# Kernel tuning notes

Hardware: AMD Instinct MI355X
Metric: run time of the kernel (lower is better)

## Reference

```python
import jax, jax.numpy as jnp
import numpy as np

B, S, D, H, MULT = 4, 2048, 768, 12, 4
HD = D // H
EPS = 1e-6


def _ln(x, g, b):
    mu = jnp.mean(x, axis=-1, keepdims=True)
    var = jnp.var(x, axis=-1, keepdims=True)
    return (x - mu) * jax.lax.rsqrt(var + EPS) * g + b


def setup_inputs() -> dict:
    key = jax.random.key(0)
    ks = jax.random.split(key, 12)
    sd = 0.02
    inp = {
        "x": jax.random.normal(ks[0], (B, S, D), dtype=jnp.float32),
        "mask": jnp.ones((B, 1, 1, S), dtype=jnp.int32),
        "Wq": jax.random.normal(ks[1], (D, D), dtype=jnp.float32) * sd,
        "bq": jnp.zeros((D,), dtype=jnp.float32),
        "Wk": jax.random.normal(ks[2], (D, D), dtype=jnp.float32) * sd,
        "bk": jnp.zeros((D,), dtype=jnp.float32),
        "Wv": jax.random.normal(ks[3], (D, D), dtype=jnp.float32) * sd,
        "bv": jnp.zeros((D,), dtype=jnp.float32),
        "Wo": jax.random.normal(ks[4], (D, D), dtype=jnp.float32) * sd,
        "bo": jnp.zeros((D,), dtype=jnp.float32),
        "W1": jax.random.normal(ks[5], (D, MULT * D), dtype=jnp.float32) * sd,
        "b1": jnp.zeros((MULT * D,), dtype=jnp.float32),
        "W2": jax.random.normal(ks[6], (MULT * D, D), dtype=jnp.float32) * sd,
        "b2": jnp.zeros((D,), dtype=jnp.float32),
        "g1": jnp.ones((D,), dtype=jnp.float32),
        "be1": jnp.zeros((D,), dtype=jnp.float32),
        "g2": jnp.ones((D,), dtype=jnp.float32),
        "be2": jnp.zeros((D,), dtype=jnp.float32),
    }
    return inp


def reference(x, mask, Wq, bq, Wk, bk, Wv, bv, Wo, bo, W1, b1, W2, b2, g1, be1, g2, be2):
    scale = HD ** -0.5
    # projections -> [B,H,S,HD]
    q = (x @ Wq + bq).reshape(B, S, H, HD).transpose(0, 2, 1, 3)
    k = (x @ Wk + bk).reshape(B, S, H, HD).transpose(0, 2, 1, 3)
    v = (x @ Wv + bv).reshape(B, S, H, HD).transpose(0, 2, 1, 3)
    scores = jnp.einsum("bhqd,bhkd->bhqk", q, k) * scale
    scores = jnp.where(mask == 0, -jnp.inf, scores)
    attn = jax.nn.softmax(scores, axis=-1)
    out = jnp.einsum("bhqk,bhkd->bhqd", attn, v)
    out = out.transpose(0, 2, 1, 3).reshape(B, S, D)
    mha = out @ Wo + bo
    # residual + LN
    h = _ln(mha + x, g1, be1)
    # FFN (dropout inactive in eval; GELU exact as torch nn.GELU default)
    ff = jax.nn.gelu(h @ W1 + b1, approximate=False) @ W2 + b2
    return _ln(ff + h, g2, be2)
```

## Files before the change

kernel.cpp:

```cpp
#include <hip/hip_runtime.h>
#include <hip/hip_bf16.h>
#include <math.h>

#define B_  4
#define S_  2048
#define D_  768
#define H_  12
#define HD_ 64
#define DF_ 3072
#define BS_ (B_*S_)

#define QSCALE 0.18033688011112042f

typedef __attribute__((ext_vector_type(8))) short short8;
typedef __attribute__((ext_vector_type(4))) float f32x4;
typedef __attribute__((ext_vector_type(4))) int  int4v;

__device__ __forceinline__ unsigned short f2b(float f){
    unsigned int x = __float_as_uint(f);
    return (unsigned short)((x + 0x7fffu + ((x >> 16) & 1u)) >> 16);
}
__device__ __forceinline__ float b2f(unsigned short u){
    return __uint_as_float(((unsigned int)u) << 16);
}

typedef __attribute__((address_space(1))) void gvoid_t;
typedef __attribute__((address_space(3))) void lvoid_t;
__device__ __forceinline__ void gload_lds16(const unsigned short* g, unsigned short* l){
    __builtin_amdgcn_global_load_lds((gvoid_t*)g, (lvoid_t*)l, 16, 0, 0);
}

__global__ __launch_bounds__(256) void prep_kernel(
    const float* __restrict__ x,
    const float* __restrict__ Wq, const float* __restrict__ Wk,
    const float* __restrict__ Wv, const float* __restrict__ Wo,
    const float* __restrict__ W1, const float* __restrict__ W2,
    const float* __restrict__ bq, const float* __restrict__ bk, const float* __restrict__ bv,
    unsigned short* __restrict__ xb, unsigned short* __restrict__ wqkvT,
    unsigned short* __restrict__ woT, unsigned short* __restrict__ w1T,
    unsigned short* __restrict__ w2T, float* __restrict__ bqkv)
{
    const int NCVT = (BS_*D_)/256;
    int bid = blockIdx.x;
    if (bid < NCVT){
        int i = bid*256 + threadIdx.x;
        xb[i] = f2b(x[i]);
        return;
    }
    bid -= NCVT;
    __shared__ float t[32][33];
    const float* src; unsigned short* dst; int K, N, bx, by;
    if (bid < 4*576){
        int wsel = bid / 576, tt = bid % 576;
        bx = tt % 24; by = tt / 24; K = D_; N = D_;
        src = (wsel==0)?Wq:(wsel==1)?Wk:(wsel==2)?Wv:Wo;
        dst = (wsel<3) ? (wqkvT + (size_t)wsel*D_*D_) : woT;
    } else if (bid < 4*576 + 2304){
        int tt = bid - 4*576; bx = tt % 96; by = tt / 96; K = D_; N = DF_; src = W1; dst = w1T;
    } else if (bid < 4*576 + 2*2304){
        int tt = bid - 4*576 - 2304; bx = tt % 24; by = tt / 24; K = DF_; N = D_; src = W2; dst = w2T;
    } else {
        int i = (bid - (4*576 + 2*2304))*256 + threadIdx.x;
        if (i < 3*D_) bqkv[i] = (i < D_) ? bq[i] : (i < 2*D_) ? bk[i-D_] : bv[i-2*D_];
        return;
    }
    int tx = threadIdx.x & 31, ty = threadIdx.x >> 5;
    #pragma unroll
    for (int i = 0; i < 4; ++i)
        t[ty + i*8][tx] = src[(size_t)(by*32 + ty + i*8) * N + bx*32 + tx];
    __syncthreads();
    #pragma unroll
    for (int i = 0; i < 4; ++i)
        dst[(size_t)(bx*32 + ty + i*8) * K + by*32 + tx] = f2b(t[tx][ty + i*8]);
}

__global__ __launch_bounds__(256, 3) void gemm_tn(
    const unsigned short* __restrict__ A,
    const unsigned short* __restrict__ Bt,
    const float* __restrict__ bias,
    float* __restrict__ Cf,
    unsigned short* __restrict__ Cb,
    unsigned short* __restrict__ vtg,
    int M, int N, int K, int klen, int act)
{
    __shared__ __align__(16) unsigned short As[128*64];
    __shared__ __align__(16) unsigned short Bs[128*64];

    const int tid  = threadIdx.x;
    const int bm   = blockIdx.y, bn = blockIdx.x, bz = blockIdx.z;
    const int w    = tid >> 6, lane = tid & 63;
    const int l16  = lane & 15, quad = lane >> 4;
    const int wm   = (w >> 1) * 64, wn = (w & 1) * 64;
    const int kbeg = bz * klen;

    const unsigned short* Abase = A  + (size_t)bm * 128 * K;
    const unsigned short* Bbase = Bt + (size_t)bn * 128 * K;

    f32x4 acc[4][4] = {};

    for (int kt = kbeg; kt < kbeg + klen; kt += 64){
        #pragma unroll
        for (int c0 = 0; c0 < 4; ++c0){
            int c = tid + c0 * 256;
            int row = c >> 3, q = c & 7;
            int sw = (q ^ row) & 7;
            gload_lds16(Abase + (size_t)row * K + kt + sw*8, As + c*8);
            gload_lds16(Bbase + (size_t)row * K + kt + sw*8, Bs + c*8);
        }
        __syncthreads();

        #pragma unroll
        for (int kc = 0; kc < 2; ++kc){
            short8 af[4], bf[4];
            #pragma unroll
            for (int mi = 0; mi < 4; ++mi)
                af[mi] = *(const short8*)&As[(wm + mi*16 + l16)*64 + (((kc*4 + quad) ^ l16) & 7)*8];
            #pragma unroll
            for (int ni = 0; ni < 4; ++ni)
                bf[ni] = *(const short8*)&Bs[(wn + ni*16 + l16)*64 + (((kc*4 + quad) ^ l16) & 7)*8];
            #pragma unroll
            for (int mi = 0; mi < 4; ++mi)
                #pragma unroll
                for (int ni = 0; ni < 4; ++ni)
                    acc[mi][ni] = __builtin_amdgcn_mfma_f32_16x16x32_bf16(af[mi], bf[ni], acc[mi][ni], 0, 0, 0);
        }
        __syncthreads();
    }

    if (act == 2 && bn >= 12){
        #pragma unroll
        for (int mi = 0; mi < 4; ++mi){
            int rowbase = bm*128 + wm + mi*16 + quad*4;
            int bidx = rowbase >> 11, s0 = rowbase & 2047;
            int sp = (s0 & ~31) | (((s0 >> 2) & 3) << 3) | (((s0 >> 4) & 1) << 2);
            #pragma unroll
            for (int ni = 0; ni < 4; ++ni){
                int col  = bn*128 + wn + ni*16 + l16;
                int hcol = col - 2*D_;
                int hh   = hcol >> 6, dd = hcol & 63;
                float bia = bias ? bias[col] : 0.f;
                unsigned long long pk = 0;
                #pragma unroll
                for (int r = 0; r < 4; ++r)
                    pk |= (unsigned long long)f2b(acc[mi][ni][r] + bia) << (16*r);
                *(unsigned long long*)(vtg + (((size_t)bidx*H_ + hh)*64 + dd)*2048 + sp) = pk;
            }
        }
        return;
    }

    float* Cfz = Cf ? (Cf + (size_t)bz * M * N) : nullptr;
    const bool addb = (bias != nullptr) && (bz == 0);
    #pragma unroll
    for (int mi = 0; mi < 4; ++mi){
        #pragma unroll
        for (int ni = 0; ni < 4; ++ni){
            int col = bn*128 + wn + ni*16 + l16;
            float bia = addb ? bias[col] : 0.f;
            #pragma unroll
            for (int r = 0; r < 4; ++r){
                int row = bm*128 + wm + mi*16 + quad*4 + r;
                float v = acc[mi][ni][r] + bia;
                if (act == 1){
                    float u = v * (0.7978845608028654f + 0.0356774081f * v * v);
                    float e = __builtin_amdgcn_exp2f(u * 2.885390081777927f);
                    v = 0.5f * v * (1.f + (1.f - 2.f / (e + 1.f)));
                } else if (act == 2 && col < D_) v *= QSCALE;
                size_t idx = (size_t)row * N + col;
                if (Cfz) Cfz[idx] = v;
                if (Cb) Cb[idx] = f2b(v);
            }
        }
    }
}

__global__ __launch_bounds__(512, 6) void attn_kernel(
    const unsigned short* __restrict__ qkv,
    const unsigned short* __restrict__ vtg,
    const int* __restrict__ mask,
    unsigned short* __restrict__ ctx)
{
    __shared__ __align__(16) unsigned short Kl[128*64];
    __shared__ __align__(16) unsigned short Vt[64*128];

    const int tid = threadIdx.x;
    const int bid = blockIdx.x;
    const int hid = bid % 48;
    const int qb  = bid / 48;
    const int h   = hid % H_;
    const int b   = hid / H_;
    const int w   = tid >> 6, lane = tid & 63;
    const int l16 = lane & 15, quad = lane >> 4;
    const int q0  = qb * 128 + w * 16;
    const size_t base = (size_t)b * S_;
    const int hoff = h * HD_;

    short8 qf[2];
    #pragma unroll
    for (int kc = 0; kc < 2; ++kc)
        qf[kc] = *(const short8*)(qkv + (base + q0 + l16)*2304 + hoff + kc*32 + quad*8);

    f32x4 o[4] = {};
    float l_s = 0.f;

    const unsigned short* vrow = vtg + ((size_t)(b*H_ + h) * 64) * 2048;

    for (int kt = 0; kt < S_/128; ++kt){
        __syncthreads();
        #pragma unroll
        for (int c0 = 0; c0 < 2; ++c0){
            int c = tid + c0*512;
            int rr = c >> 3, ch = c & 7;
            int sw = (ch ^ rr) & 7;
            gload_lds16(qkv + (base + kt*128 + rr)*2304 + D_ + hoff + sw*8, Kl + c*8);
            int d = c >> 4, pch = c & 15;
            int lch = (pch ^ d) & 15;
            gload_lds16(vrow + (size_t)d*2048 + kt*128 + lch*8, Vt + c*8);
        }
        __syncthreads();

        int mv0 = mask[b*S_ + kt*128 + lane];
        int mv1 = mask[b*S_ + kt*128 + 64 + lane];
        const bool allok = __all((mv0 != 0) && (mv1 != 0));

        #pragma unroll
        for (int t = 0; t < 4; ++t){
            f32x4 sf2[2] = {};
            #pragma unroll
            for (int kc = 0; kc < 2; ++kc){
                int co = (((kc*4 + quad) ^ l16) & 7)*8;
                short8 k0 = *(const short8*)&Kl[((2*t  )*16 + l16)*64 + co];
                short8 k1 = *(const short8*)&Kl[((2*t+1)*16 + l16)*64 + co];
                sf2[0] = __builtin_amdgcn_mfma_f32_16x16x32_bf16(k0, qf[kc], sf2[0], 0, 0, 0);
                sf2[1] = __builtin_amdgcn_mfma_f32_16x16x32_bf16(k1, qf[kc], sf2[1], 0, 0, 0);
            }
            if (!allok){
                #pragma unroll
                for (int j = 0; j < 2; ++j)
                    #pragma unroll
                    for (int r = 0; r < 4; ++r)
                        if (mask[b*S_ + kt*128 + (2*t+j)*16 + quad*4 + r] == 0)
                            sf2[j][r] = -1e30f;
            }
            #pragma unroll
            for (int j = 0; j < 2; ++j)
                #pragma unroll
                for (int r = 0; r < 4; ++r){
                    float p = __builtin_amdgcn_exp2f(sf2[j][r]);
                    sf2[j][r] = p; l_s += p;
                }
            union { unsigned int u[4]; short8 s; } pk;
            pk.u[0] = __builtin_amdgcn_perm(__float_as_uint(sf2[0][1]), __float_as_uint(sf2[0][0]), 0x07060302u);
            pk.u[1] = __builtin_amdgcn_perm(__float_as_uint(sf2[0][3]), __float_as_uint(sf2[0][2]), 0x07060302u);
            pk.u[2] = __builtin_amdgcn_perm(__float_as_uint(sf2[1][1]), __float_as_uint(sf2[1][0]), 0x07060302u);
            pk.u[3] = __builtin_amdgcn_perm(__float_as_uint(sf2[1][3]), __float_as_uint(sf2[1][2]), 0x07060302u);
            #pragma unroll
            for (int nt = 0; nt < 4; ++nt){
                int d = nt*16 + l16;
                short8 vf = *(const short8*)&Vt[d*128 + (((t*4 + quad) ^ l16) & 15)*8];
                o[nt] = __builtin_amdgcn_mfma_f32_16x16x32_bf16(pk.s, vf, o[nt], 0, 0, 0);
            }
        }
    }

    l_s += __shfl_xor(l_s, 16);
    l_s += __shfl_xor(l_s, 32);
    float linv[4];
    #pragma unroll
    for (int r = 0; r < 4; ++r)
        linv[r] = 1.f / __shfl(l_s, quad*4 + r);
    #pragma unroll
    for (int nt = 0; nt < 4; ++nt)
        #pragma unroll
        for (int r = 0; r < 4; ++r){
            int qrow = q0 + quad*4 + r;
            ctx[(base + qrow)*D_ + hoff + nt*16 + l16] = f2b(o[nt][r] * linv[r]);
        }
}

__global__ __launch_bounds__(256) void ln_kernel(
    const float* __restrict__ inp, const float* __restrict__ inp2,
    const float* __restrict__ resf, const unsigned short* __restrict__ resb,
    const float* __restrict__ g, const float* __restrict__ be,
    float* __restrict__ outf, unsigned short* __restrict__ outb)
{
    const int row = blockIdx.x;
    const int tid = threadIdx.x;
    const float* ip = inp + (size_t)row * D_;
    const float* ip2 = inp2 ? inp2 + (size_t)row * D_ : nullptr;

    float v[3], s = 0.f, ss = 0.f;
    #pragma unroll
    for (int i = 0; i < 3; ++i){
        int c = tid + i*256;
        float x = ip[c];
        if (ip2) x += ip2[c];
        x += resf ? resf[(size_t)row * D_ + c] : b2f(resb[(size_t)row * D_ + c]);
        v[i] = x; s += x; ss += x * x;
    }
    #pragma unroll
    for (int d = 1; d < 64; d <<= 1){ s += __shfl_xor(s, d); ss += __shfl_xor(ss, d); }
    __shared__ float rs[4], rss[4];
    int w = tid >> 6;
    if ((tid & 63) == 0){ rs[w] = s; rss[w] = ss; }
    __syncthreads();
    s  = rs[0] + rs[1] + rs[2] + rs[3];
    ss = rss[0] + rss[1] + rss[2] + rss[3];
    float mu   = s * (1.f / 768.f);
    float var  = ss * (1.f / 768.f) - mu * mu;
    float rstd = rsqrtf(var + 1e-6f);
    #pragma unroll
    for (int i = 0; i < 3; ++i){
        int c = tid + i*256;
        float y = (v[i] - mu) * rstd * g[c] + be[c];
        if (outf) outf[(size_t)row * D_ + c] = y;
        if (outb) outb[(size_t)row * D_ + c] = f2b(y);
    }
}

extern "C" void kernel_launch(void* const* d_in, const int* in_sizes, int n_in,
                              void* d_out, int out_size, void* d_ws, size_t ws_size,
                              hipStream_t stream)
{
    const float* x    = (const float*)d_in[0];
    const int*   mask = (const int*)  d_in[1];
    const float* Wq   = (const float*)d_in[2];
    const float* bq   = (const float*)d_in[3];
    const float* Wk   = (const float*)d_in[4];
    const float* bk   = (const float*)d_in[5];
    const float* Wv   = (const float*)d_in[6];
    const float* bv   = (const float*)d_in[7];
    const float* Wo   = (const float*)d_in[8];
    const float* bo   = (const float*)d_in[9];
    const float* W1   = (const float*)d_in[10];
    const float* b1   = (const float*)d_in[11];
    const float* W2   = (const float*)d_in[12];
    const float* b2   = (const float*)d_in[13];
    const float* g1   = (const float*)d_in[14];
    const float* be1  = (const float*)d_in[15];
    const float* g2   = (const float*)d_in[16];
    const float* be2  = (const float*)d_in[17];
    float* out = (float*)d_out;
    (void)in_sizes; (void)n_in; (void)out_size; (void)ws_size;

    char* ws = (char*)d_ws;
    const size_t n_x = (size_t)BS_ * D_;

    size_t off = 0;
    auto take = [&](size_t bytes){ size_t o = off; off += (bytes + 255) & ~(size_t)255; return o; };
    unsigned short* xb    = (unsigned short*)(ws + take(n_x * 2));
    unsigned short* hb    = xb;
    unsigned short* wqkvT = (unsigned short*)(ws + take((size_t)3*D_*D_ * 2));
    unsigned short* woT   = (unsigned short*)(ws + take((size_t)D_*D_ * 2));
    unsigned short* w1T   = (unsigned short*)(ws + take((size_t)D_*DF_ * 2));
    unsigned short* w2T   = (unsigned short*)(ws + take((size_t)D_*DF_ * 2));
    float*          bqkv  = (float*)(ws + take((size_t)3*D_ * 4));
    size_t big = take((size_t)BS_ * 2304 * 2 + n_x * 2);
    unsigned short* qkvb = (unsigned short*)(ws + big);
    unsigned short* ctxb = qkvb + (size_t)BS_ * 2304;
    unsigned short* ff1b = qkvb;
    float* pf32 = (float*)(ws + take(2 * n_x * 4));
    float* mhaf = pf32;
    float* ff2f = pf32;
    unsigned short* vtg = (unsigned short*)(ws + take(n_x * 2));

    prep_kernel<<<24576 + 3*2304 + 9, 256, 0, stream>>>(
        x, Wq, Wk, Wv, Wo, W1, W2, bq, bk, bv,
        xb, wqkvT, woT, w1T, w2T, bqkv);

    dim3 blk(256);
    gemm_tn<<<dim3(18, 64, 1), blk, 0, stream>>>(xb, wqkvT, bqkv, nullptr, qkvb, vtg, BS_, 3*D_, D_, D_, 2);
    attn_kernel<<<B_ * H_ * (S_/128), 512, 0, stream>>>(qkvb, vtg, mask, ctxb);
    gemm_tn<<<dim3(6, 64, 2), blk, 0, stream>>>(ctxb, woT, bo, mhaf, nullptr, nullptr, BS_, D_, D_, D_/2, 0);
    ln_kernel<<<BS_, blk, 0, stream>>>(mhaf, mhaf + n_x, x, nullptr, g1, be1, nullptr, hb);
    gemm_tn<<<dim3(24, 64, 1), blk, 0, stream>>>(hb, w1T, b1, nullptr, ff1b, nullptr, BS_, DF_, D_, D_, 1);
    gemm_tn<<<dim3(6, 64, 2), blk, 0, stream>>>(ff1b, w2T, b2, ff2f, nullptr, nullptr, BS_, D_, DF_, DF_/2, 0);
    ln_kernel<<<BS_, blk, 0, stream>>>(ff2f, ff2f + n_x, nullptr, hb, g2, be2, out, nullptr);
}
```

Before: 414.4 us.

## Split attention keys across warp halves with 32-row queries and LDS reduction

The attention kernel now gives each warp 32 query rows instead of 16, so every K and V fragment read from LDS feeds two MFMAs. The 128-key tile is split between two groups of four warps, whose partial outputs and row sums are combined through shared memory at the end. Output rows are staged in LDS so the context is written with coalesced 16-byte stores. Separately, the fp32-to-bf16 conversion of x in prep is vectorised to four elements per thread. The change costs more registers per thread (launch bounds drop from 6 to 4 blocks per SM) plus an extra reduction step with barriers at the end.

```diff
diff --git a/kernel.cpp b/kernel.cpp
--- a/kernel.cpp
+++ b/kernel.cpp
@@ -40,11 +40,13 @@
     unsigned short* __restrict__ woT, unsigned short* __restrict__ w1T,
     unsigned short* __restrict__ w2T, float* __restrict__ bqkv)
 {
-    const int NCVT = (BS_*D_)/256;
+    const int NCVT = (BS_*D_)/1024;
     int bid = blockIdx.x;
     if (bid < NCVT){
-        int i = bid*256 + threadIdx.x;
-        xb[i] = f2b(x[i]);
+        int i = (bid*256 + threadIdx.x)*4;
+        float4 v = *(const float4*)(x + i);
+        ushort4 o4 = { f2b(v.x), f2b(v.y), f2b(v.z), f2b(v.w) };
+        *(ushort4*)(xb + i) = o4;
         return;
     }
     bid -= NCVT;
@@ -137,13 +139,13 @@
             for (int ni = 0; ni < 4; ++ni){
                 int col  = bn*128 + wn + ni*16 + l16;
                 int hcol = col - 2*D_;
-                int hh   = hcol >> 6, dd = hcol & 63;
+                int hv   = hcol >> 6, dd = hcol & 63;
                 float bia = bias ? bias[col] : 0.f;
                 unsigned long long pk = 0;
                 #pragma unroll
                 for (int r = 0; r < 4; ++r)
                     pk |= (unsigned long long)f2b(acc[mi][ni][r] + bia) << (16*r);
-                *(unsigned long long*)(vtg + (((size_t)bidx*H_ + hh)*64 + dd)*2048 + sp) = pk;
+                *(unsigned long long*)(vtg + (((size_t)bidx*H_ + hv)*64 + dd)*2048 + sp) = pk;
             }
         }
         return;
@@ -174,14 +176,16 @@
     }
 }
 
-__global__ __launch_bounds__(512, 6) void attn_kernel(
+__global__ __launch_bounds__(512, 4) void attn_kernel(
     const unsigned short* __restrict__ qkv,
     const unsigned short* __restrict__ vtg,
     const int* __restrict__ mask,
     unsigned short* __restrict__ ctx)
 {
-    __shared__ __align__(16) unsigned short Kl[128*64];
-    __shared__ __align__(16) unsigned short Vt[64*128];
+    __shared__ __align__(16) unsigned short SMEM[128*64 + 64*128];
+    __shared__ float Ls[4][2][16];
+    unsigned short* Kl = SMEM;
+    unsigned short* Vt = SMEM + 128*64;
 
     const int tid = threadIdx.x;
     const int bid = blockIdx.x;
@@ -191,17 +195,21 @@
     const int b   = hid / H_;
     const int w   = tid >> 6, lane = tid & 63;
     const int l16 = lane & 15, quad = lane >> 4;
-    const int q0  = qb * 128 + w * 16;
+    const int wq  = w & 3;
+    const int kh  = w >> 2;
+    const int q0  = qb * 128 + wq * 32;
     const size_t base = (size_t)b * S_;
     const int hoff = h * HD_;
 
-    short8 qf[2];
-    #pragma unroll
-    for (int kc = 0; kc < 2; ++kc)
-        qf[kc] = *(const short8*)(qkv + (base + q0 + l16)*2304 + hoff + kc*32 + quad*8);
-
-    f32x4 o[4] = {};
-    float l_s = 0.f;
+    short8 qf[2][2];
+    #pragma unroll
+    for (int nq = 0; nq < 2; ++nq)
+        #pragma unroll
+        for (int kc = 0; kc < 2; ++kc)
+            qf[nq][kc] = *(const short8*)(qkv + (base + q0 + nq*16 + l16)*2304 + hoff + kc*32 + quad*8);
+
+    f32x4 o[2][4] = {};
+    float l_s[2] = {0.f, 0.f};
 
     const unsigned short* vrow = vtg + ((size_t)(b*H_ + h) * 64) * 2048;
 
@@ -219,63 +227,113 @@
         }
         __syncthreads();
 
-        int mv0 = mask[b*S_ + kt*128 + lane];
-        int mv1 = mask[b*S_ + kt*128 + 64 + lane];
-        const bool allok = __all((mv0 != 0) && (mv1 != 0));
-
-        #pragma unroll
-        for (int t = 0; t < 4; ++t){
-            f32x4 sf2[2] = {};
+        int mv = mask[b*S_ + kt*128 + kh*64 + lane];
+        const bool allok = __all(mv != 0);
+
+        #pragma unroll
+        for (int t = 0; t < 2; ++t){
+            const int tg = kh*2 + t;
+            f32x4 sf[2][2] = {};
             #pragma unroll
             for (int kc = 0; kc < 2; ++kc){
                 int co = (((kc*4 + quad) ^ l16) & 7)*8;
-                short8 k0 = *(const short8*)&Kl[((2*t  )*16 + l16)*64 + co];
-                short8 k1 = *(const short8*)&Kl[((2*t+1)*16 + l16)*64 + co];
-                sf2[0] = __builtin_amdgcn_mfma_f32_16x16x32_bf16(k0, qf[kc], sf2[0], 0, 0, 0);
-                sf2[1] = __builtin_amdgcn_mfma_f32_16x16x32_bf16(k1, qf[kc], sf2[1], 0, 0, 0);
+                short8 k0 = *(const short8*)&Kl[((2*tg  )*16 + l16)*64 + co];
+                short8 k1 = *(const short8*)&Kl[((2*tg+1)*16 + l16)*64 + co];
+                #pragma unroll
+                for (int nq = 0; nq < 2; ++nq){
+                    sf[nq][0] = __builtin_amdgcn_mfma_f32_16x16x32_bf16(k0, qf[nq][kc], sf[nq][0], 0, 0, 0);
+                    sf[nq][1] = __builtin_amdgcn_mfma_f32_16x16x32_bf16(k1, qf[nq][kc], sf[nq][1], 0, 0, 0);
+                }
             }
             if (!allok){
                 #pragma unroll
                 for (int j = 0; j < 2; ++j)
                     #pragma unroll
                     for (int r = 0; r < 4; ++r)
-                        if (mask[b*S_ + kt*128 + (2*t+j)*16 + quad*4 + r] == 0)
-                            sf2[j][r] = -1e30f;
-            }
-            #pragma unroll
-            for (int j = 0; j < 2; ++j)
-                #pragma unroll
-                for (int r = 0; r < 4; ++r){
-                    float p = __builtin_amdgcn_exp2f(sf2[j][r]);
-                    sf2[j][r] = p; l_s += p;
-                }
-            union { unsigned int u[4]; short8 s; } pk;
-            pk.u[0] = __builtin_amdgcn_perm(__float_as_uint(sf2[0][1]), __float_as_uint(sf2[0][0]), 0x07060302u);
-            pk.u[1] = __builtin_amdgcn_perm(__float_as_uint(sf2[0][3]), __float_as_uint(sf2[0][2]), 0x07060302u);
-            pk.u[2] = __builtin_amdgcn_perm(__float_as_uint(sf2[1][1]), __float_as_uint(sf2[1][0]), 0x07060302u);
-            pk.u[3] = __builtin_amdgcn_perm(__float_as_uint(sf2[1][3]), __float_as_uint(sf2[1][2]), 0x07060302u);
+                        if (mask[b*S_ + kt*128 + (2*tg+j)*16 + quad*4 + r] == 0){
+                            sf[0][j][r] = -1e30f; sf[1][j][r] = -1e30f;
+                        }
+            }
+            #pragma unroll
+            for (int nq = 0; nq < 2; ++nq)
+                #pragma unroll
+                for (int j = 0; j < 2; ++j)
+                    #pragma unroll
+                    for (int r = 0; r < 4; ++r){
+                        float p = __builtin_amdgcn_exp2f(sf[nq][j][r]);
+                        sf[nq][j][r] = p; l_s[nq] += p;
+                    }
+            short8 pf[2];
+            #pragma unroll
+            for (int nq = 0; nq < 2; ++nq){
+                union { unsigned int u[4]; short8 s; } pk;
+                pk.u[0] = __builtin_amdgcn_perm(__float_as_uint(sf[nq][0][1]), __float_as_uint(sf[nq][0][0]), 0x07060302u);
+                pk.u[1] = __builtin_amdgcn_perm(__float_as_uint(sf[nq][0][3]), __float_as_uint(sf[nq][0][2]), 0x07060302u);
+                pk.u[2] = __builtin_amdgcn_perm(__float_as_uint(sf[nq][1][1]), __float_as_uint(sf[nq][1][0]), 0x07060302u);
+                pk.u[3] = __builtin_amdgcn_perm(__float_as_uint(sf[nq][1][3]), __float_as_uint(sf[nq][1][2]), 0x07060302u);
+                pf[nq] = pk.s;
+            }
             #pragma unroll
             for (int nt = 0; nt < 4; ++nt){
                 int d = nt*16 + l16;
-                short8 vf = *(const short8*)&Vt[d*128 + (((t*4 + quad) ^ l16) & 15)*8];
-                o[nt] = __builtin_amdgcn_mfma_f32_16x16x32_bf16(pk.s, vf, o[nt], 0, 0, 0);
-            }
-        }
-    }
-
-    l_s += __shfl_xor(l_s, 16);
-    l_s += __shfl_xor(l_s, 32);
-    float linv[4];
-    #pragma unroll
-    for (int r = 0; r < 4; ++r)
-        linv[r] = 1.f / __shfl(l_s, quad*4 + r);
-    #pragma unroll
-    for (int nt = 0; nt < 4; ++nt)
-        #pragma unroll
-        for (int r = 0; r < 4; ++r){
-            int qrow = q0 + quad*4 + r;
-            ctx[(base + qrow)*D_ + hoff + nt*16 + l16] = f2b(o[nt][r] * linv[r]);
-        }
+                short8 vf = *(const short8*)&Vt[d*128 + (((tg*4 + quad) ^ l16) & 15)*8];
+                #pragma unroll
+                for (int nq = 0; nq < 2; ++nq)
+                    o[nq][nt] = __builtin_amdgcn_mfma_f32_16x16x32_bf16(pf[nq], vf, o[nq][nt], 0, 0, 0);
+            }
+        }
+    }
+
+    #pragma unroll
+    for (int nq = 0; nq < 2; ++nq){
+        l_s[nq] += __shfl_xor(l_s[nq], 16);
+        l_s[nq] += __shfl_xor(l_s[nq], 32);
+    }
+
+    float* Ol = (float*)SMEM;
+    __syncthreads();
+    if (w >= 4){
+        #pragma unroll
+        for (int nq = 0; nq < 2; ++nq){
+            #pragma unroll
+            for (int nt = 0; nt < 4; ++nt)
+                *(f32x4*)&Ol[(((w-4)*64 + lane)*32) + nq*16 + nt*4] = o[nq][nt];
+            if (quad == 0) Ls[w-4][nq][l16] = l_s[nq];
+        }
+    }
+    __syncthreads();
+    if (w < 4){
+        #pragma unroll
+        for (int nq = 0; nq < 2; ++nq){
+            #pragma unroll
+            for (int nt = 0; nt < 4; ++nt)
+                o[nq][nt] += *(const f32x4*)&Ol[((w*64 + lane)*32) + nq*16 + nt*4];
+            l_s[nq] += Ls[w][nq][l16];
+        }
+    }
+    __syncthreads();
+    if (w < 4){
+        #pragma unroll
+        for (int nq = 0; nq < 2; ++nq){
+            float linv[4];
+            #pragma unroll
+            for (int r = 0; r < 4; ++r)
+                linv[r] = 1.f / __shfl(l_s[nq], quad*4 + r);
+            #pragma unroll
+            for (int nt = 0; nt < 4; ++nt)
+                #pragma unroll
+                for (int r = 0; r < 4; ++r)
+                    SMEM[w*2048 + (nq*16 + quad*4 + r)*64 + nt*16 + l16] = f2b(o[nq][nt][r] * linv[r]);
+        }
+        asm volatile("s_waitcnt lgkmcnt(0)" ::: "memory");
+        #pragma unroll
+        for (int c0 = 0; c0 < 4; ++c0){
+            int c = lane + c0*64;
+            int qrow = c >> 3, ch = c & 7;
+            int4v vv = *(const int4v*)&SMEM[w*2048 + qrow*64 + ch*8];
+            *(int4v*)(ctx + (base + q0 + qrow)*D_ + hoff + ch*8) = vv;
+        }
+    }
 }
 
 __global__ __launch_bounds__(256) void ln_kernel(
@@ -364,7 +422,7 @@
     float* ff2f = pf32;
     unsigned short* vtg = (unsigned short*)(ws + take(n_x * 2));
 
-    prep_kernel<<<24576 + 3*2304 + 9, 256, 0, stream>>>(
+    prep_kernel<<<6144 + 3*2304 + 9, 256, 0, stream>>>(
         x, Wq, Wk, Wv, Wo, W1, W2, bq, bk, bv,
         xb, wqkvT, woT, w1T, w2T, bqkv);
 
```

Measured after the change: 423.5 us. 1.02x slower.
